# Kernel tuning notes

Hardware: AMD Instinct MI355X
Metric: run time of the kernel (lower is better)

## Reference

```python
import jax, jax.numpy as jnp
import numpy as np

CIN, HID, OUT = 128, 256, 349
NTYPES, ETYPES = 4, 5
N0, N1, N2 = 120000, 40000, 10000
GNODES, GEDGES = 250000, 2000000
E0, E1 = 1500000, 400000


def setup_inputs() -> dict:
    key = jax.random.key(0)
    ks = jax.random.split(key, 24)
    ri = jax.random.randint
    rn = jax.random.normal
    inp = {}
    inp['n_id'] = ri(ks[0], (N0,), 0, GNODES)
    inp['x0'] = rn(ks[1], (100000, CIN), dtype=jnp.float32)
    inp['src0'] = ri(ks[2], (E0,), 0, N0)
    inp['dst0'] = ri(ks[3], (E0,), 0, N1)
    inp['e_id0'] = ri(ks[4], (E0,), 0, GEDGES)
    inp['src1'] = ri(ks[5], (E1,), 0, N1)
    inp['dst1'] = ri(ks[6], (E1,), 0, N2)
    inp['e_id1'] = ri(ks[7], (E1,), 0, GEDGES)
    inp['edge_type'] = ri(ks[8], (GEDGES,), 0, ETYPES)
    inp['node_type'] = ri(ks[9], (GNODES,), 0, NTYPES)
    inp['local_node_idx'] = ri(ks[10], (GNODES,), 0, 50000)
    # learned parameters
    inp['emb1'] = rn(ks[11], (50000, CIN), dtype=jnp.float32)
    inp['emb2'] = rn(ks[12], (50000, CIN), dtype=jnp.float32)
    inp['emb3'] = rn(ks[13], (50000, CIN), dtype=jnp.float32)
    s0 = 1.0 / np.sqrt(CIN)
    s1 = 1.0 / np.sqrt(HID)
    inp['relW0'] = rn(ks[14], (ETYPES, CIN, HID), dtype=jnp.float32) * s0
    inp['rootW0'] = rn(ks[15], (NTYPES, CIN, HID), dtype=jnp.float32) * s0
    inp['rootb0'] = rn(ks[16], (NTYPES, HID), dtype=jnp.float32) * 0.02
    inp['relW1'] = rn(ks[17], (ETYPES, HID, OUT), dtype=jnp.float32) * s1
    inp['rootW1'] = rn(ks[18], (NTYPES, HID, OUT), dtype=jnp.float32) * s1
    inp['rootb1'] = rn(ks[19], (NTYPES, OUT), dtype=jnp.float32) * 0.02
    return inp


def _group_input(tables, node_type, local_node_idx, n_id):
    # RGNN.group_input: per-node-type gather from feature / embedding tables.
    nt = node_type[n_id]            # [N0]
    li = local_node_idx[n_id]       # [N0]
    h = jnp.zeros((n_id.shape[0], CIN), dtype=tables[0].dtype)
    for k, tab in enumerate(tables):
        idx = jnp.minimum(li, tab.shape[0] - 1)
        h = jnp.where((nt == k)[:, None], tab[idx], h)
    return h, nt


def _rgcn_layer(x, nt_src, src, dst, et, relW, rootW, rootb, n_tgt):
    # out = sum_t mean-aggregate(x_j over edges of type t) @ W_t  (linear commutes with mean)
    T = relW.shape[0]
    xj = x[src]                                           # [E, Cin] gather
    seg = dst * T + et                                    # fused (target, edge_type) segment id
    sums = jax.ops.segment_sum(xj, seg, num_segments=n_tgt * T)
    cnts = jax.ops.segment_sum(jnp.ones((src.shape[0],), x.dtype), seg, num_segments=n_tgt * T)
    mean = (sums / jnp.maximum(cnts, 1.0)[:, None]).reshape(n_tgt, T, -1)  # [Nt, T, Cin]
    out = jnp.einsum('ntc,tco->no', mean, relW)           # [Nt, Cout]
    # per-node-type root linear: out[mask] += root_lins[i](x_target[mask])
    x_t = x[:n_tgt]
    nt_t = nt_src[:n_tgt]
    allr = jnp.einsum('nc,tco->tno', x_t, rootW) + rootb[:, None, :]  # [Tn, Nt, Cout]
    root = jnp.take_along_axis(allr, nt_t[None, :, None], axis=0)[0]
    return out + root


def reference(n_id, x0, src0, dst0, e_id0, src1, dst1, e_id1, edge_type, node_type,
              local_node_idx, emb1, emb2, emb3, relW0, rootW0, rootb0, relW1, rootW1, rootb1):
    h, nt = _group_input([x0, emb1, emb2, emb3], node_type, local_node_idx, n_id)
    # layer 0: I -> H
    h = _rgcn_layer(h, nt, src0, dst0, edge_type[e_id0], relW0, rootW0, rootb0, N1)
    h = jax.nn.relu(h)
    nt = nt[:N1]
    # layer 1: H -> O
    h = _rgcn_layer(h, nt, src1, dst1, edge_type[e_id1], relW1, rootW1, rootb1, N2)
    return jax.nn.log_softmax(h, axis=-1)
```

## Files before the change

### kernel.cpp

```cpp
#include <hip/hip_runtime.h>
#include <hip/hip_bf16.h>
#include <cmath>

constexpr int kCIN = 128, kHID = 256, kOUT = 349;
constexpr int kNT = 4, kET = 5;
constexpr int kN0 = 120000, kN1 = 40000, kN2 = 10000;
constexpr int kNSEG0 = kN1 * kET;
constexpr int kNSEG1 = kN2 * kET;
constexpr int kNSEG = kNSEG0 + kNSEG1;

constexpr int kBinSegs = 512;
constexpr int kNBin0 = (kNSEG0 + kBinSegs - 1) / kBinSegs;
constexpr int kNBin1 = (kNSEG1 + kBinSegs - 1) / kBinSegs;
constexpr int kNBin  = kNBin0 + kNBin1;
constexpr int kNBLK  = 256;
constexpr int kSB    = 128;
constexpr int kGB    = (kN0 + 127) / 128;

typedef __bf16 bf16x8 __attribute__((ext_vector_type(8)));
typedef float f32x4 __attribute__((ext_vector_type(4)));
typedef float f32x2v __attribute__((ext_vector_type(2)));
typedef unsigned short ushort8v __attribute__((ext_vector_type(8)));

__device__ __forceinline__ unsigned short f2b(float f) {
    unsigned int b = __float_as_uint(f);
    unsigned int r = (b + 0x7FFFu + ((b >> 16) & 1u)) >> 16;
    return (unsigned short)r;
}
__device__ __forceinline__ float b2f(unsigned short u) {
    return __uint_as_float((unsigned int)u << 16);
}
__device__ __forceinline__ void gl2lds16(const void* g, void* l) {
    __builtin_amdgcn_global_load_lds(
        (const __attribute__((address_space(1))) void*)g,
        (__attribute__((address_space(3))) void*)l, 16, 0, 0);
}

__device__ __forceinline__ unsigned int f2e4m3(float f) {
#if __has_builtin(__builtin_amdgcn_cvt_pk_fp8_f32)
    return (unsigned int)(__builtin_amdgcn_cvt_pk_fp8_f32(f, f, 0, false) & 0xFF);
#else
    unsigned int sb = (__float_as_uint(f) >> 31) << 7;
    float m = fminf(fabsf(f), 448.f);
    unsigned int code;
    if (m < 0.015625f) {
        code = (unsigned int)__float2int_rn(m * 512.f);
    } else {
        unsigned int b = __float_as_uint(m);
        b = b + 0x7FFFF + ((b >> 20) & 1);
        int e8 = (int)(b >> 23) - 120;
        if (e8 > 15) code = 0x7E;
        else code = ((unsigned int)e8 << 3) | ((b >> 20) & 7);
    }
    return sb | code;
#endif
}

__device__ __forceinline__ void e4m3x4_to_f32(unsigned int u, float* o4) {
#if __has_builtin(__builtin_amdgcn_cvt_pk_f32_fp8)
    f32x2v a = __builtin_amdgcn_cvt_pk_f32_fp8(u, false);
    f32x2v b = __builtin_amdgcn_cvt_pk_f32_fp8(u, true);
    o4[0] = a[0]; o4[1] = a[1]; o4[2] = b[0]; o4[3] = b[1];
#else
#pragma unroll
    for (int i = 0; i < 4; i++) {
        unsigned int c = (u >> (8 * i)) & 0xFF;
        unsigned int s = c >> 7, e = (c >> 3) & 15, mm = c & 7;
        float v;
        if (e == 0) v = (float)mm * 0.001953125f;
        else        v = __uint_as_float((e + 120u) << 23 | mm << 20);
        o4[i] = s ? -v : v;
    }
#endif
}

__global__ void k_prep(const float* __restrict__ relW0, const float* __restrict__ rootW0,
                       unsigned short* __restrict__ Bt0T,
                       const float* __restrict__ relW1, const float* __restrict__ rootW1,
                       unsigned short* __restrict__ Bt1T,
                       const int* __restrict__ etype, unsigned char* __restrict__ et8, int nET)
{
    constexpr int T0 = kNT * 256 * 768;
    constexpr int T1 = kNT * 384 * 1536;
    constexpr int TP = T0 + T1;
    int i = blockIdx.x * 256 + threadIdx.x;
    if (i < T0) {
        int g = i / (256 * 768);
        int rem = i - g * (256 * 768);
        int col = rem / 768;
        int k = rem - col * 768;
        float v = (k < 640) ? relW0[(size_t)k * 256 + col]
                            : rootW0[((size_t)g * 128 + (k - 640)) * 256 + col];
        Bt0T[i] = f2b(v);
    } else if (i < TP) {
        int ii = i - T0;
        int g = ii / (384 * 1536);
        int rem = ii - g * (384 * 1536);
        int col = rem / 1536;
        int k = rem - col * 1536;
        float v = 0.f;
        if (col < kOUT) v = (k < 1280) ? relW1[(size_t)k * kOUT + col]
                                       : rootW1[((size_t)g * 256 + (k - 1280)) * kOUT + col];
        Bt1T[ii] = f2b(v);
    } else {
        int k = i - TP;
        if (k < nET) et8[k] = (unsigned char)etype[k];
    }
}

__global__ __launch_bounds__(1024) void k_bincnt(
    const int* __restrict__ dst0, const int* __restrict__ eid0, int E0,
    const int* __restrict__ dst1, const int* __restrict__ eid1, int E1,
    const unsigned char* __restrict__ et8, int* __restrict__ cnts2d,
    int* __restrict__ seg32,
    const int* __restrict__ n_id, const int* __restrict__ ntype, int* __restrict__ ntcnts,
    const float* __restrict__ x0, const float* __restrict__ e1f,
    const float* __restrict__ e2f, const float* __restrict__ e3f,
    const int* __restrict__ lidx,
    unsigned short* __restrict__ h0b, unsigned char* __restrict__ h0f8,
    int* __restrict__ nt0)
{
    __shared__ int h[kNBin];
    const int tid = threadIdx.x;
    if (blockIdx.x < kNBLK) {
        for (int k = tid; k < kNBin; k += 1024) h[k] = 0;
        __syncthreads();
        int Etot = E0 + E1;
        int chunk = (Etot + kNBLK - 1) / kNBLK;
        int lo = blockIdx.x * chunk;
        int hi = min(lo + chunk, Etot);
        for (int i = lo + tid; i < hi; i += 1024) {
            int c;
            if (i < E0) c = dst0[i] * kET + (int)et8[eid0[i]];
            else { int e = i - E0; c = kNBin0 * kBinSegs + dst1[e] * kET + (int)et8[eid1[e]]; }
            seg32[i] = c;
            atomicAdd(&h[c >> 9], 1);
        }
        __syncthreads();
        for (int k = tid; k < kNBin; k += 1024) cnts2d[(size_t)k * kNBLK + blockIdx.x] = h[k];
    } else if (blockIdx.x < kNBLK + 2 * kSB) {
        int b = blockIdx.x - kNBLK;
        int layer = b >= kSB;
        int blk = b - layer * kSB;
        int M = layer ? kN2 : kN1;
        if (tid < 4) h[tid] = 0;
        __syncthreads();
        int chunk = (M + kSB - 1) / kSB;
        int lo = blk * chunk, hi = min(lo + chunk, M);
        for (int i = lo + tid; i < hi; i += 1024) atomicAdd(&h[ntype[n_id[i]]], 1);
        __syncthreads();
        if (tid < 4) ntcnts[(layer * 4 + tid) * kSB + blk] = h[tid];
    } else {
        int base = (blockIdx.x - kNBLK - 2 * kSB) * 128;
        int lane = tid & 31;
        int grp = tid >> 5;
        int r[4];
        const float* tab[4];
        int idx[4], ntv[4];
        bool ok[4];
#pragma unroll
        for (int k = 0; k < 4; k++) {
            r[k] = base + grp + k * 32;
            ok[k] = r[k] < kN0;
            int rr = ok[k] ? r[k] : kN0 - 1;
            int gid = n_id[rr];
            int nt = ntype[gid];
            int li = lidx[gid];
            const float* tb; int rows;
            if (nt == 0)      { tb = x0;  rows = 100000; }
            else if (nt == 1) { tb = e1f; rows = 50000; }
            else if (nt == 2) { tb = e2f; rows = 50000; }
            else              { tb = e3f; rows = 50000; }
            tab[k] = tb;
            idx[k] = li < rows ? li : rows - 1;
            ntv[k] = nt;
        }
        float4 v[4];
#pragma unroll
        for (int k = 0; k < 4; k++)
            v[k] = reinterpret_cast<const float4*>(tab[k] + (size_t)idx[k] * kCIN)[lane];
#pragma unroll
        for (int k = 0; k < 4; k++) {
            if (!ok[k]) continue;
            unsigned int q = f2e4m3(v[k].x) | (f2e4m3(v[k].y) << 8)
                           | (f2e4m3(v[k].z) << 16) | (f2e4m3(v[k].w) << 24);
            reinterpret_cast<unsigned int*>(h0f8 + (size_t)r[k] * kCIN)[lane] = q;
            if (r[k] < kN1) {
                ushort4 o;
                o.x = f2b(v[k].x); o.y = f2b(v[k].y); o.z = f2b(v[k].z); o.w = f2b(v[k].w);
                reinterpret_cast<ushort4*>(h0b + (size_t)r[k] * kCIN)[lane] = o;
            }
            if (lane == 0) nt0[r[k]] = ntv[k];
        }
    }
}

__global__ void k_scan1(const int* __restrict__ cnt, int* __restrict__ excl,
                        int* __restrict__ blksum, int n)
{
    __shared__ int sm[1024];
    int i = blockIdx.x * 1024 + threadIdx.x;
    int v = (i < n) ? cnt[i] : 0;
    sm[threadIdx.x] = v;
    __syncthreads();
    for (int off = 1; off < 1024; off <<= 1) {
        int t = (threadIdx.x >= off) ? sm[threadIdx.x - off] : 0;
        __syncthreads();
        sm[threadIdx.x] += t;
        __syncthreads();
    }
    if (i < n) excl[i] = sm[threadIdx.x] - v;
    if (threadIdx.x == 1023) blksum[blockIdx.x] = sm[1023];
}

__global__ __launch_bounds__(1024) void k_scan2(
    int* __restrict__ blksum, int nblk,
    const int* __restrict__ ntcnts, int* __restrict__ ntoffs,
    int* __restrict__ goff0, int* __restrict__ goff1)
{
    __shared__ int sm[1024];
    int tid = threadIdx.x;
    if (blockIdx.x == 0) {
        int v = (tid < nblk) ? blksum[tid] : 0;
        sm[tid] = v;
        __syncthreads();
        for (int off = 1; off < 1024; off <<= 1) {
            int t = (tid >= off) ? sm[tid - off] : 0;
            __syncthreads();
            sm[tid] += t;
            __syncthreads();
        }
        if (tid < nblk) blksum[tid] = sm[tid] - v;
    } else {
        int v = ntcnts[tid];
        sm[tid] = v;
        __syncthreads();
        for (int off = 1; off < 512; off <<= 1) {
            int t = 0;
            if ((tid & 511) >= off) t = sm[tid - off];
            __syncthreads();
            sm[tid] += t;
            __syncthreads();
        }
        int excl = sm[tid] - v;
        ntoffs[tid] = excl;
        if ((tid & 127) == 0) {
            int layer = tid >> 9;
            int t = (tid >> 7) & 3;
            if (layer == 0) goff0[t] = excl; else goff1[t] = excl;
        }
        if (tid == 0) { goff0[4] = kN1; goff1[4] = kN2; }
    }
}

__global__ __launch_bounds__(1024) void k_binplace(
    const int* __restrict__ src0, int E0,
    const int* __restrict__ src1, int E1,
    const int* __restrict__ seg32,
    const int* __restrict__ offs2d, const int* __restrict__ blksum,
    unsigned int* __restrict__ pairs,
    const int* __restrict__ nt0, const int* __restrict__ ntoffs,
    int* __restrict__ perm0, int* __restrict__ perm1)
{
    __shared__ int cur[kNBin];
    const int tid = threadIdx.x;
    if (blockIdx.x < kNBLK) {
        for (int k = tid; k < kNBin; k += 1024) {
            size_t li = (size_t)k * kNBLK + blockIdx.x;
            cur[k] = offs2d[li] + blksum[li >> 10];
        }
        __syncthreads();
        int Etot = E0 + E1;
        int chunk = (Etot + kNBLK - 1) / kNBLK;
        int lo = blockIdx.x * chunk;
        int hi = min(lo + chunk, Etot);
        for (int i = lo + tid; i < hi; i += 1024) {
            int c = seg32[i];
            int s = (i < E0) ? src0[i] : src1[i - E0];
            unsigned int pay = (unsigned int)s | ((unsigned int)(c & (kBinSegs - 1)) << 17);
            int p = atomicAdd(&cur[c >> 9], 1);
            pairs[p] = pay;
        }
    } else {
        int b = blockIdx.x - kNBLK;
        int layer = b >= kSB;
        int blk = b - layer * kSB;
        int M = layer ? kN2 : kN1;
        int* perm = layer ? perm1 : perm0;
        if (tid < 4) cur[tid] = ntoffs[(layer * 4 + tid) * kSB + blk];
        __syncthreads();
        int chunk = (M + kSB - 1) / kSB;
        int lo = blk * chunk, hi = min(lo + chunk, M);
        for (int i = lo + tid; i < hi; i += 1024) {
            int p = atomicAdd(&cur[nt0[i]], 1);
            perm[p] = i;
        }
    }
}

__global__ __launch_bounds__(1024) void k_binscatter(
    const int* __restrict__ offs2d, const int* __restrict__ blksum, int Etot,
    const unsigned int* __restrict__ pairs,
    int* __restrict__ order, int* __restrict__ starts, int* __restrict__ cnt)
{
    __shared__ int h[kBinSegs];
    __shared__ int sc[kBinSegs];
    __shared__ int cur[kBinSegs];
    const int bin = blockIdx.x;
    const int tid = threadIdx.x;
    size_t bi = (size_t)bin * kNBLK;
    const int base = offs2d[bi] + blksum[bi >> 10];
    int end = Etot;
    if (bin + 1 < kNBin) {
        size_t ei = (size_t)(bin + 1) * kNBLK;
        end = offs2d[ei] + blksum[ei >> 10];
    }
    const int c = end - base;
    const unsigned int* pp = pairs + base;

    for (int k = tid; k < kBinSegs; k += 1024) h[k] = 0;
    __syncthreads();
    for (int j = tid; j < c; j += 1024) atomicAdd(&h[pp[j] >> 17], 1);
    __syncthreads();
    if (tid < kBinSegs) sc[tid] = h[tid];
    __syncthreads();
    for (int off = 1; off < kBinSegs; off <<= 1) {
        int t = 0;
        if (tid < kBinSegs && tid >= off) t = sc[tid - off];
        __syncthreads();
        if (tid < kBinSegs) sc[tid] += t;
        __syncthreads();
    }
    int seg_rel, abs_base, seglim;
    if (bin < kNBin0) { seg_rel = bin * kBinSegs; abs_base = seg_rel; seglim = kNSEG0 - seg_rel; }
    else { seg_rel = (bin - kNBin0) * kBinSegs; abs_base = kNSEG0 + seg_rel; seglim = kNSEG1 - seg_rel; }
    if (tid < kBinSegs) {
        int excl = sc[tid] - h[tid];
        cur[tid] = excl;
        if (tid < seglim) {
            starts[abs_base + tid] = base + excl;
            cnt[abs_base + tid] = h[tid];
        }
    }
    __syncthreads();
    for (int j = tid; j < c; j += 1024) {
        unsigned int u = pp[j];
        int sl = (int)(u >> 17);
        int p = atomicAdd(&cur[sl], 1);
        order[base + p] = (int)(u & 0x1FFFFu);
    }
}

template<int C>
__global__ __launch_bounds__(256) void k_segreduce8(
    const int* __restrict__ starts, const int* __restrict__ cnt,
    const int* __restrict__ order, const unsigned char* __restrict__ h8,
    unsigned short* __restrict__ mean, int nseg)
{
    constexpr int L = C / 16;
    constexpr int SPB = 256 / L;
    int sidx = blockIdx.x * SPB + threadIdx.x / L;
    if (sidx >= nseg) return;
    int lane = threadIdx.x % L;
    int st = starts[sidx];
    int n = cnt[sidx];
    const unsigned char* hp = h8 + (size_t)lane * 16;
    float a0[16], a1[16];
#pragma unroll
    for (int i = 0; i < 16; i++) { a0[i] = 0.f; a1[i] = 0.f; }
    int j = 0;
    for (; j + 2 <= n; j += 2) {
        int s0 = order[st + j + 0];
        int s1 = order[st + j + 1];
        uint4 u0 = *reinterpret_cast<const uint4*>(hp + (size_t)s0 * C);
        uint4 u1 = *reinterpret_cast<const uint4*>(hp + (size_t)s1 * C);
        float d[16];
        e4m3x4_to_f32(u0.x, d); e4m3x4_to_f32(u0.y, d + 4);
        e4m3x4_to_f32(u0.z, d + 8); e4m3x4_to_f32(u0.w, d + 12);
#pragma unroll
        for (int i = 0; i < 16; i++) a0[i] += d[i];
        e4m3x4_to_f32(u1.x, d); e4m3x4_to_f32(u1.y, d + 4);
        e4m3x4_to_f32(u1.z, d + 8); e4m3x4_to_f32(u1.w, d + 12);
#pragma unroll
        for (int i = 0; i < 16; i++) a1[i] += d[i];
    }
    if (j < n) {
        int s0 = order[st + j];
        uint4 u0 = *reinterpret_cast<const uint4*>(hp + (size_t)s0 * C);
        float d[16];
        e4m3x4_to_f32(u0.x, d); e4m3x4_to_f32(u0.y, d + 4);
        e4m3x4_to_f32(u0.z, d + 8); e4m3x4_to_f32(u0.w, d + 12);
#pragma unroll
        for (int i = 0; i < 16; i++) a0[i] += d[i];
    }
    float sc = 1.0f / fmaxf((float)n, 1.0f);
    ushort8v o0, o1;
#pragma unroll
    for (int i = 0; i < 8; i++) {
        o0[i] = f2b((a0[i] + a1[i]) * sc);
        o1[i] = f2b((a0[i + 8] + a1[i + 8]) * sc);
    }
    unsigned short* mp = mean + (size_t)sidx * C + lane * 16;
    *reinterpret_cast<ushort8v*>(mp) = o0;
    *reinterpret_cast<ushort8v*>(mp + 8) = o1;
}

template<int C, int BM, int BNF, int NCB, int WR, int WC, int RELU, int AF8, int OUTF32>
__global__ __launch_bounds__(256) void k_gemm_sorted(
    int M, int Nreal, int NpadK,
    const unsigned short* __restrict__ meanb,
    const unsigned short* __restrict__ hb,
    const unsigned char* __restrict__ hb8,
    const unsigned short* __restrict__ BtT,
    const float* __restrict__ rootb,
    const int* __restrict__ perm, const int* __restrict__ goff,
    float* __restrict__ outf, unsigned char* __restrict__ outf8)
{
    constexpr int K1 = kET * C;
    constexpr int K  = K1 + C;
    constexpr int FM = BM / (16 * WR);
    constexpr int FN = BNF / (16 * WC);
    __shared__ __align__(16) char ldsA[BM * 128];
    __shared__ __align__(16) char ldsB[BNF * 128];

    int nwg = gridDim.x;
    int orig = blockIdx.x;
    int q = nwg >> 3, r8 = nwg & 7, x8 = orig & 7;
    int logical = (x8 < r8 ? x8 * (q + 1) : r8 * (q + 1) + (x8 - r8) * q) + (orig >> 3);
    int colb = logical % NCB;
    int t = logical / NCB;

    int g, row0s = 0, gend = 0;
    {
        int gs[5] = {goff[0], goff[1], goff[2], goff[3], goff[4]};
        int tb = 0;
        for (g = 0; g < 4; ++g) {
            int cg = gs[g + 1] - gs[g];
            int ntl = (cg + BM - 1) / BM;
            if (t < tb + ntl) { row0s = gs[g] + (t - tb) * BM; gend = gs[g + 1]; break; }
            tb += ntl;
        }
        if (g == 4) return;
    }
    const int rows_here = min(BM, gend - row0s);
    const unsigned short* BtG = BtT + (size_t)g * NpadK;

    const int tid = threadIdx.x;
    const int col0 = colb * BNF;
    const int wid = tid >> 6, lane = tid & 63;
    const int wrow = (wid / WC) * (BM / WR);
    const int wcol = (wid % WC) * (BNF / WC);
    const int lr = lane >> 3;
    const int kb = (lane & 7) * 16;

    f32x4 acc[FM][FN] = {};

    for (int k0 = 0; k0 < K; k0 += 64) {
        const bool inMean = (k0 < K1);
        const size_t kB = (size_t)k0 * 2;
        if (!AF8 || inMean) {
#pragma unroll
            for (int c2 = 0; c2 < BM / 32; ++c2) {
                int rb = (wid * (BM / 32) + c2) * 8;
                int r = rb + lr;
                int pr = perm[row0s + min(r, rows_here - 1)];
                const char* rowp = inMean
                    ? (const char*)(meanb + (size_t)pr * K1) + kB
                    : (const char*)(hb + (size_t)pr * C) + (kB - (size_t)K1 * 2);
                gl2lds16(rowp + (kb ^ ((r & 7) << 4)), &ldsA[rb * 128]);
            }
        } else {
#pragma unroll
            for (int c2 = 0; c2 < BM / 32; ++c2) {
                int rb = (wid * (BM / 32) + c2) * 8;
                int r = rb + lr;
                int pr = perm[row0s + min(r, rows_here - 1)];
                int eo = (k0 - K1) + ((kb ^ ((r & 7) << 4)) >> 1);
                uint2 u = *reinterpret_cast<const uint2*>(hb8 + (size_t)pr * C + eo);
                float d[8];
                e4m3x4_to_f32(u.x, d); e4m3x4_to_f32(u.y, d + 4);
                ushort8v o;
#pragma unroll
                for (int i = 0; i < 8; i++) o[i] = f2b(d[i]);
                *reinterpret_cast<ushort8v*>(&ldsA[rb * 128 + lane * 16]) = o;
            }
        }
#pragma unroll
        for (int c2 = 0; c2 < BNF / 32; ++c2) {
            int rb = (wid * (BNF / 32) + c2) * 8;
            int r = rb + lr;
            const char* rowp = (const char*)(BtG + (size_t)(col0 + r) * K) + kB;
            gl2lds16(rowp + (kb ^ ((r & 7) << 4)), &ldsB[rb * 128]);
        }
        __syncthreads();
#pragma unroll
        for (int kc = 0; kc < 2; kc++) {
            int kb2 = kc * 64 + (lane >> 4) * 16;
            bf16x8 af[FM], bfr[FN];
#pragma unroll
            for (int m = 0; m < FM; m++) {
                int r = wrow + m * 16 + (lane & 15);
                af[m] = *reinterpret_cast<const bf16x8*>(&ldsA[r * 128 + (kb2 ^ ((r & 7) << 4))]);
            }
#pragma unroll
            for (int n = 0; n < FN; n++) {
                int r = wcol + n * 16 + (lane & 15);
                bfr[n] = *reinterpret_cast<const bf16x8*>(&ldsB[r * 128 + (kb2 ^ ((r & 7) << 4))]);
            }
#pragma unroll
            for (int m = 0; m < FM; m++)
#pragma unroll
                for (int n = 0; n < FN; n++)
                    acc[m][n] = __builtin_amdgcn_mfma_f32_16x16x32_bf16(af[m], bfr[n], acc[m][n], 0, 0, 0);
        }
        __syncthreads();
    }

#pragma unroll
    for (int m = 0; m < FM; m++) {
        int rlb = wrow + m * 16 + (lane >> 4) * 4;
#pragma unroll
        for (int n = 0; n < FN; n++) {
            int col = col0 + wcol + n * 16 + (lane & 15);
            if (col >= Nreal) continue;
            f32x4 v = acc[m][n];
#pragma unroll
            for (int j = 0; j < 4; j++) {
                int rl = rlb + j;
                if (rl >= rows_here) continue;
                int orig_row = perm[row0s + rl];
                float xv = v[j] + rootb[g * Nreal + col];
                if (RELU) xv = fmaxf(xv, 0.f);
                if (OUTF32) outf[(size_t)orig_row * Nreal + col] = xv;
                else        outf8[(size_t)orig_row * Nreal + col] = (unsigned char)f2e4m3(xv);
            }
        }
    }
}

__global__ void k_logsm(float* __restrict__ out, int M, int N)
{
    int row = blockIdx.x * 4 + (threadIdx.x >> 6);
    if (row >= M) return;
    int lane = threadIdx.x & 63;
    float* p = out + (size_t)row * N;
    float mx = -3.4e38f;
    for (int c = lane; c < N; c += 64) mx = fmaxf(mx, p[c]);
#pragma unroll
    for (int o = 32; o > 0; o >>= 1) mx = fmaxf(mx, __shfl_xor(mx, o));
    float s = 0.f;
    for (int c = lane; c < N; c += 64) s += expf(p[c] - mx);
#pragma unroll
    for (int o = 32; o > 0; o >>= 1) s += __shfl_xor(s, o);
    float lse = mx + logf(s);
    for (int c = lane; c < N; c += 64) p[c] -= lse;
}

extern "C" void kernel_launch(void* const* d_in, const int* in_sizes, int n_in,
                              void* d_out, int out_size, void* d_ws, size_t ws_size,
                              hipStream_t stream)
{
    const int*   n_id   = (const int*)d_in[0];
    const float* x0     = (const float*)d_in[1];
    const int*   src0   = (const int*)d_in[2];
    const int*   dst0   = (const int*)d_in[3];
    const int*   eid0   = (const int*)d_in[4];
    const int*   src1   = (const int*)d_in[5];
    const int*   dst1   = (const int*)d_in[6];
    const int*   eid1   = (const int*)d_in[7];
    const int*   etype  = (const int*)d_in[8];
    const int*   ntype  = (const int*)d_in[9];
    const int*   lidx   = (const int*)d_in[10];
    const float* emb1   = (const float*)d_in[11];
    const float* emb2   = (const float*)d_in[12];
    const float* emb3   = (const float*)d_in[13];
    const float* relW0  = (const float*)d_in[14];
    const float* rootW0 = (const float*)d_in[15];
    const float* rootb0 = (const float*)d_in[16];
    const float* relW1  = (const float*)d_in[17];
    const float* rootW1 = (const float*)d_in[18];
    const float* rootb1 = (const float*)d_in[19];
    float* out = (float*)d_out;

    const int E0 = in_sizes[2];
    const int E1 = in_sizes[5];
    const int Etot = E0 + E1;
    const int nET = in_sizes[8];
    constexpr int K0s  = kET * kCIN + kCIN;
    constexpr int K1s  = kET * kHID + kHID;
    constexpr int Npad0 = 256;
    constexpr int Npad1 = 384;

    char* ws = (char*)d_ws;
    size_t off = 0;
    auto alloc = [&](size_t bytes) -> void* {
        void* p = ws + off;
        off = (off + bytes + 255) & ~(size_t)255;
        return p;
    };
    unsigned short* h0b   = (unsigned short*)alloc((size_t)kN1 * kCIN * 2);
    unsigned char*  h0f8  = (unsigned char*)alloc((size_t)kN0 * kCIN);
    int*            nt0   = (int*)alloc((size_t)kN0 * 4);
    unsigned short* meanb = (unsigned short*)alloc((size_t)kNSEG0 * kCIN * 2);
    int*            cnt    = (int*)alloc((size_t)kNSEG * 4);
    int*            starts = (int*)alloc((size_t)kNSEG * 4);
    int*            cnts2d = (int*)alloc((size_t)kNBin * kNBLK * 4);
    int*            offs2d = (int*)alloc((size_t)kNBin * kNBLK * 4);
    int*            blksum = (int*)alloc(1024 * 4);
    unsigned int*   pairs  = (unsigned int*)alloc((size_t)Etot * 4);
    int*            order  = (int*)alloc((size_t)Etot * 4);
    int*            seg32  = (int*)alloc((size_t)Etot * 4);
    unsigned char*  et8    = (unsigned char*)alloc((size_t)nET);
    unsigned char*  h1f8  = (unsigned char*)alloc((size_t)kN1 * kHID);
    unsigned short* Bt0T  = (unsigned short*)alloc((size_t)kNT * Npad0 * K0s * 2);
    unsigned short* Bt1T  = (unsigned short*)alloc((size_t)kNT * Npad1 * K1s * 2);
    int*            perm0  = (int*)alloc((size_t)kN1 * 4);
    int*            goff0  = (int*)alloc(8 * 4);
    int*            perm1  = (int*)alloc((size_t)kN2 * 4);
    int*            goff1  = (int*)alloc(8 * 4);
    int*            ntcnts = (int*)alloc(1024 * 4);
    int*            ntoffs = (int*)alloc(1024 * 4);

    constexpr int TPREP = kNT * Npad0 * K0s + kNT * Npad1 * K1s;
    int prep_total = TPREP + nET;
    k_prep<<<(prep_total + 255) / 256, 256, 0, stream>>>(relW0, rootW0, Bt0T, relW1, rootW1, Bt1T,
                                                         etype, et8, nET);

    k_bincnt<<<kNBLK + 2 * kSB + kGB, 1024, 0, stream>>>(
        dst0, eid0, E0, dst1, eid1, E1, et8, cnts2d, seg32,
        n_id, ntype, ntcnts, x0, emb1, emb2, emb3, lidx, h0b, h0f8, nt0);

    int nscan = kNBin * kNBLK;
    int nblk = (nscan + 1023) / 1024;
    k_scan1<<<nblk, 1024, 0, stream>>>(cnts2d, offs2d, blksum, nscan);
    k_scan2<<<2, 1024, 0, stream>>>(blksum, nblk, ntcnts, ntoffs, goff0, goff1);
    k_binplace<<<kNBLK + 2 * kSB, 1024, 0, stream>>>(src0, E0, src1, E1, seg32,
                                                     offs2d, blksum, pairs, nt0, ntoffs, perm0, perm1);
    k_binscatter<<<kNBin, 1024, 0, stream>>>(offs2d, blksum, Etot, pairs, order, starts, cnt);

    k_segreduce8<kCIN><<<(kNSEG0 + 31) / 32, 256, 0, stream>>>(starts, cnt, order, h0f8, meanb, kNSEG0);
    int g0 = (kN1 / 64 + 4) * 2;
    k_gemm_sorted<kCIN, 64, 128, 2, 2, 2, 1, 0, 0><<<g0, 256, 0, stream>>>(
        kN1, kHID, Npad0 * K0s, meanb, h0b, nullptr, Bt0T, rootb0, perm0, goff0, nullptr, h1f8);

    k_segreduce8<kHID><<<(kNSEG1 + 15) / 16, 256, 0, stream>>>(starts + kNSEG0, cnt + kNSEG0, order, h1f8, meanb, kNSEG1);
    int g1 = (kN2 / 64 + 5) * 3;
    k_gemm_sorted<kHID, 64, 128, 3, 2, 2, 0, 1, 1><<<g1, 256, 0, stream>>>(
        kN2, kOUT, Npad1 * K1s, meanb, nullptr, h1f8, Bt1T, rootb1, perm1, goff1, out, nullptr);

    k_logsm<<<(kN2 + 3) / 4, 256, 0, stream>>>(out, kN2, kOUT);
}
```

Measured before the change: 218.0 us.

## Fuse layer-0 bin scatter with segment mean reduction using LDS-resident order

The bin-scatter kernel now keeps each bin's sorted source indices in shared memory. For layer-0 bins it computes the fp8 gather-and-mean directly from that LDS order, which removes the separate layer-0 segreduce launch and the global write and reread of order, starts and cnt. The gather/root-block section of k_bincnt is also moved to the front of the grid. In exchange, each block of 512 threads handles 512 segments in 8 sequential passes, so there are far fewer parallel gather streams. Bins holding more than 8192 edges would silently drop entries.

```diff
diff --git a/kernel.cpp b/kernel.cpp
--- a/kernel.cpp
+++ b/kernel.cpp
@@ -16,6 +16,7 @@
 constexpr int kNBLK  = 256;
 constexpr int kSB    = 128;
 constexpr int kGB    = (kN0 + 127) / 128;
+constexpr int kBinCap = 8192;
 
 typedef __bf16 bf16x8 __attribute__((ext_vector_type(8)));
 typedef float f32x4 __attribute__((ext_vector_type(4)));
@@ -122,36 +123,8 @@
 {
     __shared__ int h[kNBin];
     const int tid = threadIdx.x;
-    if (blockIdx.x < kNBLK) {
-        for (int k = tid; k < kNBin; k += 1024) h[k] = 0;
-        __syncthreads();
-        int Etot = E0 + E1;
-        int chunk = (Etot + kNBLK - 1) / kNBLK;
-        int lo = blockIdx.x * chunk;
-        int hi = min(lo + chunk, Etot);
-        for (int i = lo + tid; i < hi; i += 1024) {
-            int c;
-            if (i < E0) c = dst0[i] * kET + (int)et8[eid0[i]];
-            else { int e = i - E0; c = kNBin0 * kBinSegs + dst1[e] * kET + (int)et8[eid1[e]]; }
-            seg32[i] = c;
-            atomicAdd(&h[c >> 9], 1);
-        }
-        __syncthreads();
-        for (int k = tid; k < kNBin; k += 1024) cnts2d[(size_t)k * kNBLK + blockIdx.x] = h[k];
-    } else if (blockIdx.x < kNBLK + 2 * kSB) {
-        int b = blockIdx.x - kNBLK;
-        int layer = b >= kSB;
-        int blk = b - layer * kSB;
-        int M = layer ? kN2 : kN1;
-        if (tid < 4) h[tid] = 0;
-        __syncthreads();
-        int chunk = (M + kSB - 1) / kSB;
-        int lo = blk * chunk, hi = min(lo + chunk, M);
-        for (int i = lo + tid; i < hi; i += 1024) atomicAdd(&h[ntype[n_id[i]]], 1);
-        __syncthreads();
-        if (tid < 4) ntcnts[(layer * 4 + tid) * kSB + blk] = h[tid];
-    } else {
-        int base = (blockIdx.x - kNBLK - 2 * kSB) * 128;
+    if (blockIdx.x < kGB) {
+        int base = blockIdx.x * 128;
         int lane = tid & 31;
         int grp = tid >> 5;
         int r[4];
@@ -192,6 +165,35 @@
             }
             if (lane == 0) nt0[r[k]] = ntv[k];
         }
+    } else if (blockIdx.x < kGB + kNBLK) {
+        int blk = blockIdx.x - kGB;
+        for (int k = tid; k < kNBin; k += 1024) h[k] = 0;
+        __syncthreads();
+        int Etot = E0 + E1;
+        int chunk = (Etot + kNBLK - 1) / kNBLK;
+        int lo = blk * chunk;
+        int hi = min(lo + chunk, Etot);
+        for (int i = lo + tid; i < hi; i += 1024) {
+            int c;
+            if (i < E0) c = dst0[i] * kET + (int)et8[eid0[i]];
+            else { int e = i - E0; c = kNBin0 * kBinSegs + dst1[e] * kET + (int)et8[eid1[e]]; }
+            seg32[i] = c;
+            atomicAdd(&h[c >> 9], 1);
+        }
+        __syncthreads();
+        for (int k = tid; k < kNBin; k += 1024) cnts2d[(size_t)k * kNBLK + blk] = h[k];
+    } else {
+        int b = blockIdx.x - kGB - kNBLK;
+        int layer = b >= kSB;
+        int blk = b - layer * kSB;
+        int M = layer ? kN2 : kN1;
+        if (tid < 4) h[tid] = 0;
+        __syncthreads();
+        int chunk = (M + kSB - 1) / kSB;
+        int lo = blk * chunk, hi = min(lo + chunk, M);
+        for (int i = lo + tid; i < hi; i += 1024) atomicAdd(&h[ntype[n_id[i]]], 1);
+        __syncthreads();
+        if (tid < 4) ntcnts[(layer * 4 + tid) * kSB + blk] = h[tid];
     }
 }
 
@@ -298,14 +300,16 @@
     }
 }
 
-__global__ __launch_bounds__(1024) void k_binscatter(
+__global__ __launch_bounds__(512) void k_binseg(
     const int* __restrict__ offs2d, const int* __restrict__ blksum, int Etot,
     const unsigned int* __restrict__ pairs,
-    int* __restrict__ order, int* __restrict__ starts, int* __restrict__ cnt)
+    int* __restrict__ order, int* __restrict__ starts, int* __restrict__ cnt,
+    const unsigned char* __restrict__ h0f8, unsigned short* __restrict__ meanb)
 {
     __shared__ int h[kBinSegs];
     __shared__ int sc[kBinSegs];
     __shared__ int cur[kBinSegs];
+    __shared__ int ordl[kBinCap];
     const int bin = blockIdx.x;
     const int tid = threadIdx.x;
     size_t bi = (size_t)bin * kNBLK;
@@ -318,36 +322,87 @@
     const int c = end - base;
     const unsigned int* pp = pairs + base;
 
-    for (int k = tid; k < kBinSegs; k += 1024) h[k] = 0;
+    h[tid] = 0;
     __syncthreads();
-    for (int j = tid; j < c; j += 1024) atomicAdd(&h[pp[j] >> 17], 1);
+    for (int j = tid; j < c; j += 512) atomicAdd(&h[pp[j] >> 17], 1);
     __syncthreads();
-    if (tid < kBinSegs) sc[tid] = h[tid];
+    sc[tid] = h[tid];
     __syncthreads();
     for (int off = 1; off < kBinSegs; off <<= 1) {
-        int t = 0;
-        if (tid < kBinSegs && tid >= off) t = sc[tid - off];
-        __syncthreads();
-        if (tid < kBinSegs) sc[tid] += t;
-        __syncthreads();
-    }
-    int seg_rel, abs_base, seglim;
-    if (bin < kNBin0) { seg_rel = bin * kBinSegs; abs_base = seg_rel; seglim = kNSEG0 - seg_rel; }
-    else { seg_rel = (bin - kNBin0) * kBinSegs; abs_base = kNSEG0 + seg_rel; seglim = kNSEG1 - seg_rel; }
-    if (tid < kBinSegs) {
-        int excl = sc[tid] - h[tid];
-        cur[tid] = excl;
-        if (tid < seglim) {
-            starts[abs_base + tid] = base + excl;
-            cnt[abs_base + tid] = h[tid];
-        }
-    }
+        int t = (tid >= off) ? sc[tid - off] : 0;
+        __syncthreads();
+        sc[tid] += t;
+        __syncthreads();
+    }
+    cur[tid] = sc[tid] - h[tid];
     __syncthreads();
-    for (int j = tid; j < c; j += 1024) {
+    for (int j = tid; j < c; j += 512) {
         unsigned int u = pp[j];
         int sl = (int)(u >> 17);
         int p = atomicAdd(&cur[sl], 1);
-        order[base + p] = (int)(u & 0x1FFFFu);
+        if (p < kBinCap) ordl[p] = (int)(u & 0x1FFFFu);
+    }
+    __syncthreads();
+
+    if (bin < kNBin0) {
+        int seg_base = bin * kBinSegs;
+        int seglim = min(kBinSegs, kNSEG0 - seg_base);
+#pragma unroll 1
+        for (int pass = 0; pass < 8; ++pass) {
+            int srel = (tid >> 3) + pass * 64;
+            if (srel >= seglim) continue;
+            int lane = tid & 7;
+            int st = sc[srel] - h[srel];
+            int n = h[srel];
+            const unsigned char* hp = h0f8 + (size_t)lane * 16;
+            float a0[16], a1[16];
+#pragma unroll
+            for (int i = 0; i < 16; i++) { a0[i] = 0.f; a1[i] = 0.f; }
+            int j = 0;
+            for (; j + 2 <= n; j += 2) {
+                int s0 = ordl[st + j];
+                int s1 = ordl[st + j + 1];
+                uint4 u0 = *reinterpret_cast<const uint4*>(hp + (size_t)s0 * kCIN);
+                uint4 u1 = *reinterpret_cast<const uint4*>(hp + (size_t)s1 * kCIN);
+                float d[16];
+                e4m3x4_to_f32(u0.x, d); e4m3x4_to_f32(u0.y, d + 4);
+                e4m3x4_to_f32(u0.z, d + 8); e4m3x4_to_f32(u0.w, d + 12);
+#pragma unroll
+                for (int i = 0; i < 16; i++) a0[i] += d[i];
+                e4m3x4_to_f32(u1.x, d); e4m3x4_to_f32(u1.y, d + 4);
+                e4m3x4_to_f32(u1.z, d + 8); e4m3x4_to_f32(u1.w, d + 12);
+#pragma unroll
+                for (int i = 0; i < 16; i++) a1[i] += d[i];
+            }
+            if (j < n) {
+                int s0 = ordl[st + j];
+                uint4 u0 = *reinterpret_cast<const uint4*>(hp + (size_t)s0 * kCIN);
+                float d[16];
+                e4m3x4_to_f32(u0.x, d); e4m3x4_to_f32(u0.y, d + 4);
+                e4m3x4_to_f32(u0.z, d + 8); e4m3x4_to_f32(u0.w, d + 12);
+#pragma unroll
+                for (int i = 0; i < 16; i++) a0[i] += d[i];
+            }
+            float scv = 1.0f / fmaxf((float)n, 1.0f);
+            ushort8v o0, o1;
+#pragma unroll
+            for (int i = 0; i < 8; i++) {
+                o0[i] = f2b((a0[i] + a1[i]) * scv);
+                o1[i] = f2b((a0[i + 8] + a1[i + 8]) * scv);
+            }
+            unsigned short* mp = meanb + (size_t)(seg_base + srel) * kCIN + lane * 16;
+            *reinterpret_cast<ushort8v*>(mp) = o0;
+            *reinterpret_cast<ushort8v*>(mp + 8) = o1;
+        }
+    } else {
+        int seg_rel = (bin - kNBin0) * kBinSegs;
+        int abs_base = kNSEG0 + seg_rel;
+        int seglim = kNSEG1 - seg_rel;
+        if (tid < seglim) {
+            starts[abs_base + tid] = base + (sc[tid] - h[tid]);
+            cnt[abs_base + tid] = h[tid];
+        }
+        for (int j = tid; j < c; j += 512) order[base + j] = ordl[j];
     }
 }
 
@@ -626,7 +681,7 @@
     k_prep<<<(prep_total + 255) / 256, 256, 0, stream>>>(relW0, rootW0, Bt0T, relW1, rootW1, Bt1T,
                                                          etype, et8, nET);
 
-    k_bincnt<<<kNBLK + 2 * kSB + kGB, 1024, 0, stream>>>(
+    k_bincnt<<<kGB + kNBLK + 2 * kSB, 1024, 0, stream>>>(
         dst0, eid0, E0, dst1, eid1, E1, et8, cnts2d, seg32,
         n_id, ntype, ntcnts, x0, emb1, emb2, emb3, lidx, h0b, h0f8, nt0);
 
@@ -636,9 +691,10 @@
     k_scan2<<<2, 1024, 0, stream>>>(blksum, nblk, ntcnts, ntoffs, goff0, goff1);
     k_binplace<<<kNBLK + 2 * kSB, 1024, 0, stream>>>(src0, E0, src1, E1, seg32,
                                                      offs2d, blksum, pairs, nt0, ntoffs, perm0, perm1);
-    k_binscatter<<<kNBin, 1024, 0, stream>>>(offs2d, blksum, Etot, pairs, order, starts, cnt);
-
-    k_segreduce8<kCIN><<<(kNSEG0 + 31) / 32, 256, 0, stream>>>(starts, cnt, order, h0f8, meanb, kNSEG0);
+
+    k_binseg<<<kNBin, 512, 0, stream>>>(offs2d, blksum, Etot, pairs, order, starts, cnt,
+                                        h0f8, meanb);
+
     int g0 = (kN1 / 64 + 4) * 2;
     k_gemm_sorted<kCIN, 64, 128, 2, 2, 2, 1, 0, 0><<<g0, 256, 0, stream>>>(
         kN1, kHID, Npad0 * K0s, meanb, h0b, nullptr, Bt0T, rootb0, perm0, goff0, nullptr, h1f8);
```

Result: no change. 219.0 us (+0.5%).
